# Optimization experiments

Measured on AMD Instinct MI355X. Metric: run time of the kernel, lower is better.

## Reference

```python
import jax, jax.numpy as jnp
import numpy as np

B, S, D = 8, 1024, 1024
H = 16
HD = D // H
FFN = 4096
BN = 64  # adapter bottleneck
ADAPTER_SCALE = 0.1
EPS = 1e-5


def _ln(x, g, b):
    m = jnp.mean(x, axis=-1, keepdims=True)
    v = jnp.mean(jnp.square(x - m), axis=-1, keepdims=True)
    return (x - m) * jax.lax.rsqrt(v + EPS) * g + b


def setup_inputs() -> dict:
    key = jax.random.key(0)
    ks = jax.random.split(key, 16)
    sd = 0.02
    # weights stored [in, out] (math identical to torch's x @ W.T with W [out,in])
    return {
        "x": jax.random.normal(ks[0], (B, S, D), jnp.float32),
        "ln1_g": jnp.ones((D,), jnp.float32),
        "ln1_b": jnp.zeros((D,), jnp.float32),
        "wq": jax.random.normal(ks[1], (D, D), jnp.float32) * sd,
        "wk": jax.random.normal(ks[2], (D, D), jnp.float32) * sd,
        "wv": jax.random.normal(ks[3], (D, D), jnp.float32) * sd,
        "wo": jax.random.normal(ks[4], (D, D), jnp.float32) * sd,
        "bo": jnp.zeros((D,), jnp.float32),
        "ln2_g": jnp.ones((D,), jnp.float32),
        "ln2_b": jnp.zeros((D,), jnp.float32),
        "w1": jax.random.normal(ks[5], (D, FFN), jnp.float32) * sd,
        "b1": jnp.zeros((FFN,), jnp.float32),
        "w2": jax.random.normal(ks[6], (FFN, D), jnp.float32) * sd,
        "b2": jnp.zeros((D,), jnp.float32),
        "aln_g": jnp.ones((D,), jnp.float32),
        "aln_b": jnp.zeros((D,), jnp.float32),
        "wd": jax.random.normal(ks[7], (D, BN), jnp.float32) * sd,
        "bd": jnp.zeros((BN,), jnp.float32),
        "wu": jax.random.normal(ks[8], (BN, D), jnp.float32) * sd,
        "bu": jnp.zeros((D,), jnp.float32),
    }


def reference(x, ln1_g, ln1_b, wq, wk, wv, wo, bo, ln2_g, ln2_b,
              w1, b1, w2, b2, aln_g, aln_b, wd, bd, wu, bu):
    b, s, d = x.shape
    scale = HD ** -0.5

    # --- attention branch ---
    h = _ln(x, ln1_g, ln1_b)
    q = (h @ wq).reshape(b, s, H, HD)
    k = (h @ wk).reshape(b, s, H, HD)
    v = (h @ wv).reshape(b, s, H, HD)
    scores = jnp.einsum('bqhd,bkhd->bhqk', q, k) * scale  # [B,H,S,S]
    probs = jax.nn.softmax(scores, axis=-1)
    attn = jnp.einsum('bhqk,bkhd->bqhd', probs, v).reshape(b, s, d)
    x = x + (attn @ wo + bo)

    # --- parallel adapter (LN-in, down-relu-up, scaled, no residual) ---
    a = _ln(x, aln_g, aln_b)
    adapt_x = (jax.nn.relu(a @ wd + bd) @ wu + bu) * ADAPTER_SCALE

    # --- MLP branch ---
    residual = x
    h2 = _ln(x, ln2_g, ln2_b)
    h2 = jax.nn.gelu(h2 @ w1 + b1, approximate=False)
    h2 = h2 @ w2 + b2
    h2 = h2 + adapt_x
    return residual + h2
```

## Files before the change

### kernel.cpp

```cpp
#include <hip/hip_runtime.h>
#include <hip/hip_bf16.h>
#include <cstdint>
#include <cstddef>

#define DI __device__ __forceinline__

typedef __attribute__((ext_vector_type(8))) short v8s;
typedef __attribute__((ext_vector_type(4))) float v4f;
typedef __attribute__((ext_vector_type(16))) float v16f;

DI void gload_lds16(const unsigned short* g, unsigned short* l) {
  __builtin_amdgcn_global_load_lds(
      (const __attribute__((address_space(1))) unsigned int*)g,
      (__attribute__((address_space(3))) unsigned int*)l, 16, 0, 0);
}

DI float bf2f(unsigned short u) { return __uint_as_float(((unsigned int)u) << 16); }
DI unsigned short f2bf(float f) {
  unsigned int u = __float_as_uint(f);
  u += 0x7FFFu + ((u >> 16) & 1u);
  return (unsigned short)(u >> 16);
}

__global__ __launch_bounds__(256) void transpose_cvt_k(
    const float* __restrict__ in, unsigned short* __restrict__ out, int R, int C) {
  __shared__ unsigned short t[32][33];
  const int j0 = blockIdx.x * 32, i0 = blockIdx.y * 32;
  const int tx = threadIdx.x & 31, ty = threadIdx.x >> 5;
#pragma unroll
  for (int r = 0; r < 32; r += 8) t[ty + r][tx] = f2bf(in[(size_t)(i0 + ty + r) * C + j0 + tx]);
  __syncthreads();
#pragma unroll
  for (int r = 0; r < 32; r += 8) out[(size_t)(j0 + ty + r) * R + i0 + tx] = t[tx][ty + r];
}

__global__ __launch_bounds__(256) void vtrans_k(
    const unsigned short* __restrict__ v, unsigned short* __restrict__ vt, int ld) {
  __shared__ unsigned short t[32][33];
  const int bh = blockIdx.z, b = bh >> 4, h = bh & 15;
  const int s0 = blockIdx.x * 32, d0 = blockIdx.y * 32;
  const int tx = threadIdx.x & 31, ty = threadIdx.x >> 5;
  const unsigned short* src = v + (size_t)(b * 1024 + s0) * ld + h * 64 + d0;
#pragma unroll
  for (int r = 0; r < 32; r += 8) t[ty + r][tx] = src[(size_t)(ty + r) * ld + tx];
  __syncthreads();
  unsigned short* dst = vt + ((size_t)bh * 64 + d0) * 1024 + s0;
#pragma unroll
  for (int r = 0; r < 32; r += 8) dst[(size_t)(ty + r) * 1024 + tx] = t[tx][ty + r];
}

__global__ __launch_bounds__(256) void ln_k(
    const float* __restrict__ x, const float* __restrict__ g,
    const float* __restrict__ b, unsigned short* __restrict__ out) {
  const int row = blockIdx.x;
  const float4 v = ((const float4*)(x + (size_t)row * 1024))[threadIdx.x];
  float s = v.x + v.y + v.z + v.w;
  float ss = v.x * v.x + v.y * v.y + v.z * v.z + v.w * v.w;
#pragma unroll
  for (int o = 1; o < 64; o <<= 1) { s += __shfl_xor(s, o); ss += __shfl_xor(ss, o); }
  __shared__ float red[8];
  const int wid = threadIdx.x >> 6, lane = threadIdx.x & 63;
  if (!lane) { red[wid] = s; red[4 + wid] = ss; }
  __syncthreads();
  s = red[0] + red[1] + red[2] + red[3];
  ss = red[4] + red[5] + red[6] + red[7];
  const float mean = s * (1.f / 1024.f);
  const float var = ss * (1.f / 1024.f) - mean * mean;
  const float rs = rsqrtf(var + 1e-5f);
  const float4 gv = ((const float4*)g)[threadIdx.x];
  const float4 bv = ((const float4*)b)[threadIdx.x];
  ushort4 ov;
  ov.x = f2bf((v.x - mean) * rs * gv.x + bv.x);
  ov.y = f2bf((v.y - mean) * rs * gv.y + bv.y);
  ov.z = f2bf((v.z - mean) * rs * gv.z + bv.z);
  ov.w = f2bf((v.w - mean) * rs * gv.w + bv.w);
  ((ushort4*)(out + (size_t)row * 1024))[threadIdx.x] = ov;
}

__global__ __launch_bounds__(256) void ln_dual_k(
    const float* __restrict__ x, const float* __restrict__ g1, const float* __restrict__ b1,
    const float* __restrict__ g2, const float* __restrict__ b2,
    unsigned short* __restrict__ o1, unsigned short* __restrict__ o2) {
  const int row = blockIdx.x;
  const float4 v = ((const float4*)(x + (size_t)row * 1024))[threadIdx.x];
  float s = v.x + v.y + v.z + v.w;
  float ss = v.x * v.x + v.y * v.y + v.z * v.z + v.w * v.w;
#pragma unroll
  for (int o = 1; o < 64; o <<= 1) { s += __shfl_xor(s, o); ss += __shfl_xor(ss, o); }
  __shared__ float red[8];
  const int wid = threadIdx.x >> 6, lane = threadIdx.x & 63;
  if (!lane) { red[wid] = s; red[4 + wid] = ss; }
  __syncthreads();
  s = red[0] + red[1] + red[2] + red[3];
  ss = red[4] + red[5] + red[6] + red[7];
  const float mean = s * (1.f / 1024.f);
  const float var = ss * (1.f / 1024.f) - mean * mean;
  const float rs = rsqrtf(var + 1e-5f);
  const float n0 = (v.x - mean) * rs, n1 = (v.y - mean) * rs, n2 = (v.z - mean) * rs, n3 = (v.w - mean) * rs;
  {
    const float4 gv = ((const float4*)g1)[threadIdx.x];
    const float4 bv = ((const float4*)b1)[threadIdx.x];
    ushort4 ov{f2bf(n0 * gv.x + bv.x), f2bf(n1 * gv.y + bv.y), f2bf(n2 * gv.z + bv.z), f2bf(n3 * gv.w + bv.w)};
    ((ushort4*)(o1 + (size_t)row * 1024))[threadIdx.x] = ov;
  }
  {
    const float4 gv = ((const float4*)g2)[threadIdx.x];
    const float4 bv = ((const float4*)b2)[threadIdx.x];
    ushort4 ov{f2bf(n0 * gv.x + bv.x), f2bf(n1 * gv.y + bv.y), f2bf(n2 * gv.z + bv.z), f2bf(n3 * gv.w + bv.w)};
    ((ushort4*)(o2 + (size_t)row * 1024))[threadIdx.x] = ov;
  }
}

enum { EPI_NONE = 0, EPI_BIAS_RES = 1, EPI_GELU = 2, EPI_RELU = 3, EPI_SCALE_BIAS = 4, EPI_FINAL = 5 };

template <int BM, int BN, int EPI, typename CT>
__global__ __launch_bounds__(512, 2) void gemm8_k(
    const unsigned short* __restrict__ A, const unsigned short* __restrict__ Bt,
    CT* __restrict__ C, const float* __restrict__ bias,
    const float* __restrict__ res, const float* __restrict__ extra,
    int M, int N, int K, int gm, int gn) {
  constexpr int MF = BM / 32, NF = BN / 64;
  constexpr int PH = (MF * NF) / 8 < 1 ? 1 : (MF * NF) / 8;
  constexpr int MPP = MF / PH;
  constexpr int LA = BM / 64, LB = BN / 64, LT = LA + LB;
  constexpr int BUFE = (BM + BN) * 64;
  __shared__ unsigned short lds[BUFE * 2];
  const int tid = threadIdx.x;
  const int lane = tid & 63, wid = tid >> 6;
  const int wm = wid >> 2, wn = wid & 3;
  const int l15 = lane & 15, l4 = lane >> 4;
  const int nwg = gm * gn;
  const int bid = blockIdx.x;
  const int swz = (bid % 8) * (nwg / 8) + bid / 8;
  const int row0 = (swz / gn) * BM, col0 = (swz % gn) * BN;
  const int NT = K >> 6;

  const int srow = tid >> 3, sgr = tid & 7;
  auto stA = [&](int kt, int b, int a) {
    const unsigned short* s = A + (size_t)(row0 + a * 64 + srow) * K + kt * 64 + ((sgr ^ (srow & 7)) << 3);
    gload_lds16(s, lds + b * BUFE + a * 4096 + tid * 8);
  };
  auto stB = [&](int kt, int b, int a) {
    const unsigned short* s = Bt + (size_t)(col0 + a * 64 + srow) * K + kt * 64 + ((sgr ^ (srow & 7)) << 3);
    gload_lds16(s, lds + b * BUFE + BM * 64 + a * 4096 + tid * 8);
  };

#pragma unroll
  for (int e = 0; e < LA; ++e) stA(0, 0, e);
#pragma unroll
  for (int e = 0; e < LB; ++e) stB(0, 0, e);
  if (NT > 1) {
#pragma unroll
    for (int e = 0; e < LB; ++e) stB(1, 1, e);
    asm volatile("s_waitcnt vmcnt(%0)" ::"n"(LB) : "memory");
  } else {
    asm volatile("s_waitcnt vmcnt(0)" ::: "memory");
  }
  __builtin_amdgcn_s_barrier();

  v4f acc[MF][NF] = {};
  v8s bfr[NF][2];
  for (int t = 0; t < NT; ++t) {
    const int buf = t & 1;
    const unsigned short* La = lds + buf * BUFE;
    const unsigned short* Lb = lds + buf * BUFE + BM * 64;
#pragma unroll
    for (int p = 0; p < PH; ++p) {
      if (p == 0) {
#pragma unroll
        for (int nf = 0; nf < NF; ++nf) {
          const int r = wn * (BN / 4) + nf * 16 + l15;
#pragma unroll
          for (int kk = 0; kk < 2; ++kk)
            bfr[nf][kk] = *(const v8s*)(Lb + r * 64 + ((kk * 32 + l4 * 8) ^ ((r & 7) << 3)));
        }
      }
      v8s af[MPP][2];
#pragma unroll
      for (int mm = 0; mm < MPP; ++mm) {
        const int r = wm * (BM / 2) + (p * MPP + mm) * 16 + l15;
#pragma unroll
        for (int kk = 0; kk < 2; ++kk)
          af[mm][kk] = *(const v8s*)(La + r * 64 + ((kk * 32 + l4 * 8) ^ ((r & 7) << 3)));
      }
#pragma unroll
      for (int e = p * LT / PH; e < (p + 1) * LT / PH; ++e) {
        if (e < LA) { if (t + 1 < NT) stA(t + 1, buf ^ 1, e); }
        else        { if (t + 2 < NT) stB(t + 2, buf, e - LA); }
      }
      __builtin_amdgcn_s_barrier();
      asm volatile("s_waitcnt lgkmcnt(0)" ::: "memory");
      __builtin_amdgcn_s_setprio(1);
#pragma unroll
      for (int mm = 0; mm < MPP; ++mm)
#pragma unroll
        for (int nf = 0; nf < NF; ++nf)
#pragma unroll
          for (int kk = 0; kk < 2; ++kk)
            acc[p * MPP + mm][nf] = __builtin_amdgcn_mfma_f32_16x16x32_bf16(
                af[mm][kk], bfr[nf][kk], acc[p * MPP + mm][nf], 0, 0, 0);
      __builtin_amdgcn_s_setprio(0);
      if (p == PH - 1 && t + 1 < NT) {
        if (t + 2 < NT) asm volatile("s_waitcnt vmcnt(%0)" ::"n"(LB) : "memory");
        else            asm volatile("s_waitcnt vmcnt(0)" ::: "memory");
      }
      __builtin_amdgcn_s_barrier();
    }
  }

#pragma unroll
  for (int mf = 0; mf < MF; ++mf) {
#pragma unroll
    for (int nf = 0; nf < NF; ++nf) {
      const int col = col0 + wn * (BN / 4) + nf * 16 + l15;
      float bv = 0.f;
      if (EPI != EPI_NONE) bv = bias[col];
#pragma unroll
      for (int j = 0; j < 4; ++j) {
        const int row = row0 + wm * (BM / 2) + mf * 16 + l4 * 4 + j;
        const size_t idx = (size_t)row * N + col;
        float v = acc[mf][nf][j];
        if (EPI == EPI_BIAS_RES) v += bv + res[idx];
        else if (EPI == EPI_GELU) { v += bv; v = 0.5f * v * (1.f + erff(v * 0.70710678118f)); }
        else if (EPI == EPI_RELU) { v += bv; v = fmaxf(v, 0.f); }
        else if (EPI == EPI_SCALE_BIAS) { v = (v + bv) * 0.1f; }
        else if (EPI == EPI_FINAL) { v += bv + res[idx] + extra[idx]; }
        if constexpr (sizeof(CT) == 2) C[idx] = f2bf(v); else C[idx] = v;
      }
    }
  }
}

template <int BN, int EPI, typename CT>
__global__ __launch_bounds__(256) void gemm_k(
    const unsigned short* __restrict__ A, const unsigned short* __restrict__ Bt,
    CT* __restrict__ C, const float* __restrict__ bias,
    const float* __restrict__ res, const float* __restrict__ extra,
    int M, int N, int K) {
  constexpr int BM = 128, BK = 32;
  constexpr int WN = (BN == 128) ? 2 : 1;
  constexpr int MR = (BN == 128) ? 4 : 2;
  constexpr int NR = 4;
  __shared__ unsigned short sA[BM * BK];
  __shared__ unsigned short sB[BN * BK];
  const int tid = threadIdx.x;
  const int lane = tid & 63, wid = tid >> 6;
  const int wm = wid / WN, wn = wid % WN;
  const int l15 = lane & 15, l4 = lane >> 4;
  const int row0 = blockIdx.x * BM, col0 = blockIdx.y * BN;
  v4f acc[MR][NR] = {};
  const int rowA = wm * MR * 16;
  const int rowB = wn * NR * 16;
  for (int k0 = 0; k0 < K; k0 += BK) {
#pragma unroll
    for (int r = 0; r < (BM * BK) / (256 * 8); ++r) {
      int e = (r * 256 + tid) * 8;
      gload_lds16(A + (size_t)(row0 + (e >> 5)) * K + k0 + (e & 31), ((unsigned short*)sA) + e);
    }
#pragma unroll
    for (int r = 0; r < (BN * BK) / (256 * 8); ++r) {
      int e = (r * 256 + tid) * 8;
      gload_lds16(Bt + (size_t)(col0 + (e >> 5)) * K + k0 + (e & 31), ((unsigned short*)sB) + e);
    }
    __syncthreads();
    v8s af[MR], bfr2[NR];
#pragma unroll
    for (int m = 0; m < MR; ++m) af[m] = *(const v8s*)(sA + (rowA + m * 16 + l15) * BK + l4 * 8);
#pragma unroll
    for (int n = 0; n < NR; ++n) bfr2[n] = *(const v8s*)(sB + (rowB + n * 16 + l15) * BK + l4 * 8);
#pragma unroll
    for (int m = 0; m < MR; ++m)
#pragma unroll
      for (int n = 0; n < NR; ++n)
        acc[m][n] = __builtin_amdgcn_mfma_f32_16x16x32_bf16(af[m], bfr2[n], acc[m][n], 0, 0, 0);
    __syncthreads();
  }
#pragma unroll
  for (int m = 0; m < MR; ++m) {
#pragma unroll
    for (int n = 0; n < NR; ++n) {
      const int col = col0 + rowB + n * 16 + l15;
      float bv = 0.f;
      if (EPI != EPI_NONE) bv = bias[col];
#pragma unroll
      for (int j = 0; j < 4; ++j) {
        const int row = row0 + rowA + m * 16 + l4 * 4 + j;
        const size_t idx = (size_t)row * N + col;
        float v = acc[m][n][j];
        if (EPI == EPI_BIAS_RES) v += bv + res[idx];
        else if (EPI == EPI_GELU) { v += bv; v = 0.5f * v * (1.f + erff(v * 0.70710678118f)); }
        else if (EPI == EPI_RELU) { v += bv; v = fmaxf(v, 0.f); }
        else if (EPI == EPI_SCALE_BIAS) { v = (v + bv) * 0.1f; }
        else if (EPI == EPI_FINAL) { v += bv + res[idx] + extra[idx]; }
        if constexpr (sizeof(CT) == 2) C[idx] = f2bf(v); else C[idx] = v;
      }
    }
  }
}

__global__ __launch_bounds__(256) void attn_k(
    const unsigned short* __restrict__ QKV, const unsigned short* __restrict__ VT,
    unsigned short* __restrict__ O) {
  const int bid = blockIdx.x;
  const int swz = (bid & 7) * 128 + (bid >> 3);
  const int bh = swz >> 3, qb = swz & 7;
  const int b = bh >> 4, h = bh & 15;
  const int tid = threadIdx.x, lane = tid & 63, w = tid >> 6;
  const int l31 = lane & 31, hi = lane >> 5;
  __shared__ unsigned short sK[2][64 * 64];
  __shared__ unsigned short sV[2][64 * 64];
  const int q0 = qb * 128;
  const unsigned short* Qrow = QKV + (size_t)(b * 1024 + q0 + w * 32 + l31) * 3072 + h * 64;
  v8s qf[4];
#pragma unroll
  for (int kcd = 0; kcd < 4; ++kcd) qf[kcd] = *(const v8s*)(Qrow + kcd * 16 + hi * 8);

  const unsigned short* Kbase = QKV + 1024 + (size_t)(b * 1024) * 3072 + h * 64;
  const unsigned short* Vbase = VT + (size_t)bh * 64 * 1024;
  const int sr = tid >> 3, sg = tid & 7;
  auto stage = [&](int t, int bsel) {
    const int k0 = t * 64;
#pragma unroll
    for (int ps = 0; ps < 2; ++ps) {
      const int r = ps * 32 + sr;
      gload_lds16(Kbase + (size_t)(k0 + r) * 3072 + ((sg ^ (r & 7)) << 3), &sK[bsel][r * 64 + sg * 8]);
    }
#pragma unroll
    for (int ps = 0; ps < 2; ++ps) {
      const int r = ps * 32 + sr;
      gload_lds16(Vbase + (size_t)r * 1024 + k0 + ((sg ^ (r & 7)) << 3), &sV[bsel][r * 64 + sg * 8]);
    }
  };
  stage(0, 0);
  asm volatile("s_waitcnt vmcnt(0)" ::: "memory");
  __syncthreads();

  const float SC = 0.125f * 1.44269504f;
  float m_run = -3e38f, l_run = 0.f;
  v16f oacc0 = {}, oacc1 = {};

  for (int t = 0; t < 16; ++t) {
    const int cur = t & 1;
    if (t + 1 < 16) stage(t + 1, cur ^ 1);
    v16f s0 = {}, s1 = {};
#pragma unroll
    for (int kcd = 0; kcd < 4; ++kcd) {
      const int c = kcd * 2 + hi;
      v8s a0 = *(const v8s*)(&sK[cur][l31 * 64 + ((c ^ (l31 & 7)) << 3)]);
      v8s a1 = *(const v8s*)(&sK[cur][(32 + l31) * 64 + ((c ^ (l31 & 7)) << 3)]);
      s0 = __builtin_amdgcn_mfma_f32_32x32x16_bf16(a0, qf[kcd], s0, 0, 0, 0);
      s1 = __builtin_amdgcn_mfma_f32_32x32x16_bf16(a1, qf[kcd], s1, 0, 0, 0);
    }
    float p0[16], p1[16];
#pragma unroll
    for (int i = 0; i < 16; ++i) { p0[i] = s0[i] * SC; p1[i] = s1[i] * SC; }
    float mx = fmaxf(p0[0], p1[0]);
#pragma unroll
    for (int i = 1; i < 16; ++i) mx = fmaxf(mx, fmaxf(p0[i], p1[i]));
    mx = fmaxf(mx, __shfl_xor(mx, 32));
    const float m_new = fmaxf(m_run, mx);
    const float fac = exp2f(m_run - m_new);
    float ts = 0.f;
#pragma unroll
    for (int i = 0; i < 16; ++i) {
      p0[i] = exp2f(p0[i] - m_new);
      p1[i] = exp2f(p1[i] - m_new);
      ts += p0[i] + p1[i];
    }
    ts += __shfl_xor(ts, 32);
    l_run = l_run * fac + ts;
    m_run = m_new;
#pragma unroll
    for (int i = 0; i < 16; ++i) { oacc0[i] *= fac; oacc1[i] *= fac; }
    auto mkfrag = [&](const float* p, int c) -> v8s {
      unsigned A0, A1, A2, A3;
      asm("v_cvt_pk_bf16_f32 %0, %1, %2" : "=v"(A0) : "v"(p[8 * c + 0]), "v"(p[8 * c + 1]));
      asm("v_cvt_pk_bf16_f32 %0, %1, %2" : "=v"(A1) : "v"(p[8 * c + 2]), "v"(p[8 * c + 3]));
      asm("v_cvt_pk_bf16_f32 %0, %1, %2" : "=v"(A2) : "v"(p[8 * c + 4]), "v"(p[8 * c + 5]));
      asm("v_cvt_pk_bf16_f32 %0, %1, %2" : "=v"(A3) : "v"(p[8 * c + 6]), "v"(p[8 * c + 7]));
      asm("v_permlane32_swap_b32 %0, %1" : "+v"(A2), "+v"(A0));
      asm("v_permlane32_swap_b32 %0, %1" : "+v"(A3), "+v"(A1));
      union { unsigned u[4]; v8s v; } r;
      r.u[0] = A0; r.u[1] = A1; r.u[2] = A2; r.u[3] = A3;
      return r.v;
    };
    v8s pB0 = mkfrag(p0, 0), pB1 = mkfrag(p0, 1), pB2 = mkfrag(p1, 0), pB3 = mkfrag(p1, 1);
#pragma unroll
    for (int kc = 0; kc < 4; ++kc) {
      const v8s pb = (kc == 0) ? pB0 : (kc == 1) ? pB1 : (kc == 2) ? pB2 : pB3;
      const int c = kc * 2 + hi;
      v8s vf0 = *(const v8s*)(&sV[cur][l31 * 64 + ((c ^ (l31 & 7)) << 3)]);
      v8s vf1 = *(const v8s*)(&sV[cur][(32 + l31) * 64 + ((c ^ (l31 & 7)) << 3)]);
      oacc0 = __builtin_amdgcn_mfma_f32_32x32x16_bf16(vf0, pb, oacc0, 0, 0, 0);
      oacc1 = __builtin_amdgcn_mfma_f32_32x32x16_bf16(vf1, pb, oacc1, 0, 0, 0);
    }
    if (t + 1 < 16) {
      asm volatile("s_waitcnt vmcnt(0)" ::: "memory");
      __syncthreads();
    }
  }
  const float inv = 1.f / l_run;
  unsigned short* Orow = O + (size_t)(b * 1024 + q0 + w * 32 + l31) * 1024 + h * 64;
#pragma unroll
  for (int g = 0; g < 4; ++g) {
    ushort4 st0{f2bf(oacc0[4 * g + 0] * inv), f2bf(oacc0[4 * g + 1] * inv),
                f2bf(oacc0[4 * g + 2] * inv), f2bf(oacc0[4 * g + 3] * inv)};
    ushort4 st1{f2bf(oacc1[4 * g + 0] * inv), f2bf(oacc1[4 * g + 1] * inv),
                f2bf(oacc1[4 * g + 2] * inv), f2bf(oacc1[4 * g + 3] * inv)};
    *(ushort4*)(Orow + g * 8 + hi * 4) = st0;
    *(ushort4*)(Orow + 32 + g * 8 + hi * 4) = st1;
  }
}

extern "C" void kernel_launch(void* const* d_in, const int* in_sizes, int n_in,
                              void* d_out, int out_size, void* d_ws, size_t ws_size,
                              hipStream_t stream) {
  (void)in_sizes; (void)n_in; (void)out_size;
  const float* x    = (const float*)d_in[0];
  const float* ln1g = (const float*)d_in[1];
  const float* ln1b = (const float*)d_in[2];
  const float* wq   = (const float*)d_in[3];
  const float* wk   = (const float*)d_in[4];
  const float* wv   = (const float*)d_in[5];
  const float* wo   = (const float*)d_in[6];
  const float* bo   = (const float*)d_in[7];
  const float* ln2g = (const float*)d_in[8];
  const float* ln2b = (const float*)d_in[9];
  const float* w1   = (const float*)d_in[10];
  const float* b1   = (const float*)d_in[11];
  const float* w2   = (const float*)d_in[12];
  const float* b2   = (const float*)d_in[13];
  const float* alng = (const float*)d_in[14];
  const float* alnb = (const float*)d_in[15];
  const float* wd   = (const float*)d_in[16];
  const float* bd   = (const float*)d_in[17];
  const float* wu   = (const float*)d_in[18];
  const float* bu   = (const float*)d_in[19];
  float* out = (float*)d_out;

  char* W = (char*)d_ws;
  size_t off = 0;
  auto allocB = [&](size_t bytes) { void* p = W + off; off += (bytes + 255) & ~(size_t)255; return p; };
  const size_t T = 8192;
  unsigned short* wqkvt = (unsigned short*)allocB((size_t)3072 * 1024 * 2);
  unsigned short* wot   = (unsigned short*)allocB((size_t)1024 * 1024 * 2);
  unsigned short* w1t   = (unsigned short*)allocB((size_t)4096 * 1024 * 2);
  unsigned short* w2t   = (unsigned short*)allocB((size_t)4096 * 1024 * 2);
  unsigned short* wdt   = (unsigned short*)allocB(64 * 1024 * 2);
  unsigned short* wut   = (unsigned short*)allocB(64 * 1024 * 2);
  unsigned short* H     = (unsigned short*)allocB(T * 1024 * 2);
  unsigned short* H2    = (unsigned short*)allocB(T * 1024 * 2);
  unsigned short* QKV   = (unsigned short*)allocB(T * 3072 * 2);
  unsigned short* VT    = (unsigned short*)allocB(T * 1024 * 2);
  float* X2             = (float*)allocB(T * 1024 * 4);
  unsigned short* MID   = (unsigned short*)allocB(T * 4096 * 2);
  unsigned short* AO  = MID;
  unsigned short* DWN = VT;
  float* ADP          = (float*)QKV;
  if (ws_size < off) return;

  dim3 blk(256);
  transpose_cvt_k<<<dim3(32, 32), blk, 0, stream>>>(wq, wqkvt, 1024, 1024);
  transpose_cvt_k<<<dim3(32, 32), blk, 0, stream>>>(wk, wqkvt + (size_t)1024 * 1024, 1024, 1024);
  transpose_cvt_k<<<dim3(32, 32), blk, 0, stream>>>(wv, wqkvt + (size_t)2048 * 1024, 1024, 1024);
  transpose_cvt_k<<<dim3(32, 32), blk, 0, stream>>>(wo, wot, 1024, 1024);
  transpose_cvt_k<<<dim3(128, 32), blk, 0, stream>>>(w1, w1t, 1024, 4096);
  transpose_cvt_k<<<dim3(32, 128), blk, 0, stream>>>(w2, w2t, 4096, 1024);
  transpose_cvt_k<<<dim3(2, 32), blk, 0, stream>>>(wd, wdt, 1024, 64);
  transpose_cvt_k<<<dim3(32, 2), blk, 0, stream>>>(wu, wut, 64, 1024);

  ln_k<<<8192, blk, 0, stream>>>(x, ln1g, ln1b, H);
  gemm8_k<128, 256, EPI_NONE, unsigned short><<<768, 512, 0, stream>>>(
      H, wqkvt, QKV, nullptr, nullptr, nullptr, 8192, 3072, 1024, 64, 12);
  vtrans_k<<<dim3(32, 2, 128), blk, 0, stream>>>(QKV + 2048, VT, 3072);
  attn_k<<<1024, blk, 0, stream>>>(QKV, VT, AO);
  gemm8_k<128, 256, EPI_BIAS_RES, float><<<256, 512, 0, stream>>>(
      AO, wot, X2, bo, x, nullptr, 8192, 1024, 1024, 64, 4);
  ln_dual_k<<<8192, blk, 0, stream>>>(X2, alng, alnb, ln2g, ln2b, H, H2);
  gemm_k<64, EPI_RELU, unsigned short><<<dim3(64, 1), blk, 0, stream>>>(
      H, wdt, DWN, bd, nullptr, nullptr, 8192, 64, 1024);
  gemm_k<128, EPI_SCALE_BIAS, float><<<dim3(64, 8), blk, 0, stream>>>(
      DWN, wut, ADP, bu, nullptr, nullptr, 8192, 1024, 64);
  gemm8_k<256, 256, EPI_GELU, unsigned short><<<512, 512, 0, stream>>>(
      H2, w1t, MID, b1, nullptr, nullptr, 8192, 4096, 1024, 32, 16);
  gemm8_k<128, 256, EPI_FINAL, float><<<256, 512, 0, stream>>>(
      MID, w2t, out, b2, X2, ADP, 8192, 1024, 4096, 64, 4);
}
```

Baseline: 570.4 us.

## Use fast erf in GELU, reschedule GEMM prefetch and MFMA order, hoist addresses

Replaces erff in the GELU epilogues with an Abramowitz-Stegun polynomial that uses a hardware reciprocal and a fast exp. In the GEMM main loop, all A-tile prefetches are now issued in phase 0 and the B-tile prefetches are spread over the later phases, and the MFMA loop is reordered so the k-chunk is the outer loop. Global load addresses are precomputed and advanced incrementally in both the GEMM and attention kernels to cut integer address arithmetic. The attention kernel also raises wave priority around its MFMA blocks. The erf approximation is accurate to about 1e-7 absolute, and the changed prefetch split alters the memory overlap pattern.

Result: faster. 550.3 us (-3.5%).

```diff
diff --git a/kernel.cpp b/kernel.cpp
--- a/kernel.cpp
+++ b/kernel.cpp
@@ -20,6 +20,15 @@
   unsigned int u = __float_as_uint(f);
   u += 0x7FFFu + ((u >> 16) & 1u);
   return (unsigned short)(u >> 16);
+}
+
+DI float fast_erf(float x) {
+  const float ax = fabsf(x);
+  const float t = __builtin_amdgcn_rcpf(1.f + 0.3275911f * ax);
+  const float y = t * (0.254829592f + t * (-0.284496736f + t * (1.421413741f +
+                   t * (-1.453152027f + t * 1.061405429f))));
+  const float r = 1.f - y * __expf(-ax * ax);
+  return copysignf(r, x);
 }
 
 __global__ __launch_bounds__(256) void transpose_cvt_k(
@@ -122,7 +131,7 @@
   constexpr int MF = BM / 32, NF = BN / 64;
   constexpr int PH = (MF * NF) / 8 < 1 ? 1 : (MF * NF) / 8;
   constexpr int MPP = MF / PH;
-  constexpr int LA = BM / 64, LB = BN / 64, LT = LA + LB;
+  constexpr int LA = BM / 64, LB = BN / 64;
   constexpr int BUFE = (BM + BN) * 64;
   __shared__ unsigned short lds[BUFE * 2];
   const int tid = threadIdx.x;
@@ -136,13 +145,17 @@
   const int NT = K >> 6;
 
   const int srow = tid >> 3, sgr = tid & 7;
-  auto stA = [&](int kt, int b, int a) {
-    const unsigned short* s = A + (size_t)(row0 + a * 64 + srow) * K + kt * 64 + ((sgr ^ (srow & 7)) << 3);
-    gload_lds16(s, lds + b * BUFE + a * 4096 + tid * 8);
+  const unsigned short* Atb = A + (size_t)(row0 + srow) * K + ((sgr ^ (srow & 7)) << 3);
+  const unsigned short* Btb = Bt + (size_t)(col0 + srow) * K + ((sgr ^ (srow & 7)) << 3);
+  const size_t eStr = (size_t)64 * K;
+  unsigned short* ldsA = lds + tid * 8;
+  unsigned short* ldsB = lds + BM * 64 + tid * 8;
+
+  auto stA = [&](int kt, int b, int e) {
+    gload_lds16(Atb + (size_t)e * eStr + kt * 64, ldsA + b * BUFE + e * 4096);
   };
-  auto stB = [&](int kt, int b, int a) {
-    const unsigned short* s = Bt + (size_t)(col0 + a * 64 + srow) * K + kt * 64 + ((sgr ^ (srow & 7)) << 3);
-    gload_lds16(s, lds + b * BUFE + BM * 64 + a * 4096 + tid * 8);
+  auto stB = [&](int kt, int b, int e) {
+    gload_lds16(Btb + (size_t)e * eStr + kt * 64, ldsB + b * BUFE + e * 4096);
   };
 
 #pragma unroll
@@ -183,20 +196,27 @@
         for (int kk = 0; kk < 2; ++kk)
           af[mm][kk] = *(const v8s*)(La + r * 64 + ((kk * 32 + l4 * 8) ^ ((r & 7) << 3)));
       }
-#pragma unroll
-      for (int e = p * LT / PH; e < (p + 1) * LT / PH; ++e) {
-        if (e < LA) { if (t + 1 < NT) stA(t + 1, buf ^ 1, e); }
-        else        { if (t + 2 < NT) stB(t + 2, buf, e - LA); }
+      if (p == 0) {
+        if (t + 1 < NT) {
+#pragma unroll
+          for (int e = 0; e < LA; ++e) stA(t + 1, buf ^ 1, e);
+        }
+      } else {
+        if (t + 2 < NT) {
+          constexpr int BPP = (LB + PH - 2) / (PH - 1 > 0 ? PH - 1 : 1);
+#pragma unroll
+          for (int e = (p - 1) * BPP; e < p * BPP && e < LB; ++e) stB(t + 2, buf, e);
+        }
       }
       __builtin_amdgcn_s_barrier();
       asm volatile("s_waitcnt lgkmcnt(0)" ::: "memory");
       __builtin_amdgcn_s_setprio(1);
 #pragma unroll
-      for (int mm = 0; mm < MPP; ++mm)
-#pragma unroll
-        for (int nf = 0; nf < NF; ++nf)
-#pragma unroll
-          for (int kk = 0; kk < 2; ++kk)
+      for (int kk = 0; kk < 2; ++kk)
+#pragma unroll
+        for (int mm = 0; mm < MPP; ++mm)
+#pragma unroll
+          for (int nf = 0; nf < NF; ++nf)
             acc[p * MPP + mm][nf] = __builtin_amdgcn_mfma_f32_16x16x32_bf16(
                 af[mm][kk], bfr[nf][kk], acc[p * MPP + mm][nf], 0, 0, 0);
       __builtin_amdgcn_s_setprio(0);
@@ -221,7 +241,7 @@
         const size_t idx = (size_t)row * N + col;
         float v = acc[mf][nf][j];
         if (EPI == EPI_BIAS_RES) v += bv + res[idx];
-        else if (EPI == EPI_GELU) { v += bv; v = 0.5f * v * (1.f + erff(v * 0.70710678118f)); }
+        else if (EPI == EPI_GELU) { v += bv; v = 0.5f * v * (1.f + fast_erf(v * 0.70710678118f)); }
         else if (EPI == EPI_RELU) { v += bv; v = fmaxf(v, 0.f); }
         else if (EPI == EPI_SCALE_BIAS) { v = (v + bv) * 0.1f; }
         else if (EPI == EPI_FINAL) { v += bv + res[idx] + extra[idx]; }
@@ -288,7 +308,7 @@
         const size_t idx = (size_t)row * N + col;
         float v = acc[m][n][j];
         if (EPI == EPI_BIAS_RES) v += bv + res[idx];
-        else if (EPI == EPI_GELU) { v += bv; v = 0.5f * v * (1.f + erff(v * 0.70710678118f)); }
+        else if (EPI == EPI_GELU) { v += bv; v = 0.5f * v * (1.f + fast_erf(v * 0.70710678118f)); }
         else if (EPI == EPI_RELU) { v += bv; v = fmaxf(v, 0.f); }
         else if (EPI == EPI_SCALE_BIAS) { v = (v + bv) * 0.1f; }
         else if (EPI == EPI_FINAL) { v += bv + res[idx] + extra[idx]; }
@@ -318,20 +338,23 @@
   const unsigned short* Kbase = QKV + 1024 + (size_t)(b * 1024) * 3072 + h * 64;
   const unsigned short* Vbase = VT + (size_t)bh * 64 * 1024;
   const int sr = tid >> 3, sg = tid & 7;
-  auto stage = [&](int t, int bsel) {
-    const int k0 = t * 64;
-#pragma unroll
-    for (int ps = 0; ps < 2; ++ps) {
-      const int r = ps * 32 + sr;
-      gload_lds16(Kbase + (size_t)(k0 + r) * 3072 + ((sg ^ (r & 7)) << 3), &sK[bsel][r * 64 + sg * 8]);
-    }
-#pragma unroll
-    for (int ps = 0; ps < 2; ++ps) {
-      const int r = ps * 32 + sr;
-      gload_lds16(Vbase + (size_t)r * 1024 + k0 + ((sg ^ (r & 7)) << 3), &sV[bsel][r * 64 + sg * 8]);
-    }
+  const unsigned short* kp0 = Kbase + (size_t)sr * 3072 + ((sg ^ (sr & 7)) << 3);
+  const unsigned short* kp1 = Kbase + (size_t)(32 + sr) * 3072 + ((sg ^ (sr & 7)) << 3);
+  const unsigned short* vp0 = Vbase + (size_t)sr * 1024 + ((sg ^ (sr & 7)) << 3);
+  const unsigned short* vp1 = Vbase + (size_t)(32 + sr) * 1024 + ((sg ^ (sr & 7)) << 3);
+  unsigned short* dK0 = &sK[0][sr * 64 + sg * 8];
+  unsigned short* dK1 = &sK[0][(32 + sr) * 64 + sg * 8];
+  unsigned short* dV0 = &sV[0][sr * 64 + sg * 8];
+  unsigned short* dV1 = &sV[0][(32 + sr) * 64 + sg * 8];
+  constexpr int BOFF = 64 * 64;
+  auto stage = [&](int bsel) {
+    gload_lds16(kp0, dK0 + bsel * BOFF);
+    gload_lds16(kp1, dK1 + bsel * BOFF);
+    gload_lds16(vp0, dV0 + bsel * BOFF);
+    gload_lds16(vp1, dV1 + bsel * BOFF);
+    kp0 += (size_t)64 * 3072; kp1 += (size_t)64 * 3072; vp0 += 64; vp1 += 64;
   };
-  stage(0, 0);
+  stage(0);
   asm volatile("s_waitcnt vmcnt(0)" ::: "memory");
   __syncthreads();
 
@@ -341,8 +364,9 @@
 
   for (int t = 0; t < 16; ++t) {
     const int cur = t & 1;
-    if (t + 1 < 16) stage(t + 1, cur ^ 1);
+    if (t + 1 < 16) stage(cur ^ 1);
     v16f s0 = {}, s1 = {};
+    __builtin_amdgcn_s_setprio(1);
 #pragma unroll
     for (int kcd = 0; kcd < 4; ++kcd) {
       const int c = kcd * 2 + hi;
@@ -351,6 +375,7 @@
       s0 = __builtin_amdgcn_mfma_f32_32x32x16_bf16(a0, qf[kcd], s0, 0, 0, 0);
       s1 = __builtin_amdgcn_mfma_f32_32x32x16_bf16(a1, qf[kcd], s1, 0, 0, 0);
     }
+    __builtin_amdgcn_s_setprio(0);
     float p0[16], p1[16];
 #pragma unroll
     for (int i = 0; i < 16; ++i) { p0[i] = s0[i] * SC; p1[i] = s1[i] * SC; }
@@ -385,6 +410,7 @@
       return r.v;
     };
     v8s pB0 = mkfrag(p0, 0), pB1 = mkfrag(p0, 1), pB2 = mkfrag(p1, 0), pB3 = mkfrag(p1, 1);
+    __builtin_amdgcn_s_setprio(1);
 #pragma unroll
     for (int kc = 0; kc < 4; ++kc) {
       const v8s pb = (kc == 0) ? pB0 : (kc == 1) ? pB1 : (kc == 2) ? pB2 : pB3;
@@ -394,6 +420,7 @@
       oacc0 = __builtin_amdgcn_mfma_f32_32x32x16_bf16(vf0, pb, oacc0, 0, 0, 0);
       oacc1 = __builtin_amdgcn_mfma_f32_32x32x16_bf16(vf1, pb, oacc1, 0, 0, 0);
     }
+    __builtin_amdgcn_s_setprio(0);
     if (t + 1 < 16) {
       asm volatile("s_waitcnt vmcnt(0)" ::: "memory");
       __syncthreads();
```
